# Kernel tuning notes

Measured on AMD Instinct MI355X. Metric: run time of the kernel, lower is better.

Reference implementation:

```python
import jax, jax.numpy as jnp
import numpy as np

B, S, E, FEAT, ATT, NCLS, VOCAB = 32, 512, 512, 256, 10, 8, 32000
# NOTE: original code requires S == E (attentive_content [S,S] assigned into a [S,E] buffer)


def setup_inputs() -> dict:
    key = jax.random.key(0)
    ks = jax.random.split(key, 8)
    x = jax.random.randint(ks[0], (B, S), 0, VOCAB)
    emb = jax.random.normal(ks[1], (VOCAB, E), dtype=jnp.float32) * 0.02
    A = jax.random.uniform(ks[2], (E, ATT), dtype=jnp.float32, minval=-0.1, maxval=0.1)
    Wh = jax.random.normal(ks[3], (FEAT, E, 3), dtype=jnp.float32) * 0.02   # h_conv, k=3, no bias
    Wc = jax.random.normal(ks[4], (FEAT, E), dtype=jnp.float32) * 0.02      # c_conv, k=1, no bias
    tanh_bias = jnp.zeros((FEAT,), dtype=jnp.float32)
    Wfc = jax.random.normal(ks[5], (NCLS, FEAT), dtype=jnp.float32) * 0.02
    bfc = jnp.zeros((NCLS,), dtype=jnp.float32)
    return {"x": x, "emb": emb, "A": A, "Wh": Wh, "Wc": Wc,
            "tanh_bias": tanh_bias, "Wfc": Wfc, "bfc": bfc}


def reference(x, emb, A, Wh, Wc, tanh_bias, Wfc, bfc):
    ex = emb[x]                                    # [B,S,E] embedding lookup
    # batched version of the per-sample loop: mm -> softmax -> mm
    scores = jnp.einsum('bse,ea->bsa', ex, A)      # [B,S,ATT]
    attn = jax.nn.softmax(scores, axis=-1)         # softmax over attention dim (2D default)
    att = jnp.einsum('bsa,bta->bst', attn, scores)  # [B,S,S]  (S == E)
    # h branch: conv1d(k=3, valid) over time, then global max-pool
    h = jax.lax.conv_general_dilated(ex.transpose(0, 2, 1), Wh, (1,), 'VALID',
                                     dimension_numbers=('NCH', 'OIH', 'NCH'))  # [B,F,S-2]
    h = jnp.max(h, axis=-1)                        # [B,F]
    # c branch: k=1 conv over att (permuted), i.e. channel mix, then global max-pool
    c = jnp.max(jnp.einsum('blc,fc->bfl', att, Wc), axis=-1)  # [B,F]
    out = jnp.tanh(h + c + tanh_bias)
    return out @ Wfc.T + bfc                       # [B,num_class]
```

## Files before the change

### kernel.cpp

```cpp
#include <hip/hip_runtime.h>
#include <math.h>

#define B 32
#define S 512
#define E 512
#define FEAT 256
#define ATT 10
#define NCLS 8

using short8 = __attribute__((ext_vector_type(8))) short;
using f32x4  = __attribute__((ext_vector_type(4))) float;

__device__ __forceinline__ unsigned short f2bf(float f) {
    unsigned int u = __float_as_uint(f);
    return (unsigned short)((u + 0x7fffu + ((u >> 16) & 1u)) >> 16);
}

__device__ __forceinline__ void gl16(const void* g, void* l) {
    __builtin_amdgcn_global_load_lds(
        (const __attribute__((address_space(1))) unsigned int*)g,
        (__attribute__((address_space(3))) unsigned int*)l, 16, 0, 0);
}

__global__ __launch_bounds__(256) void k_front(
        const int* __restrict__ x, const float* __restrict__ emb,
        const float* __restrict__ A, const float* __restrict__ Wh,
        unsigned short* __restrict__ ex16, unsigned short* __restrict__ Whk16,
        float* __restrict__ sc12, float* __restrict__ at12) {
    const int blk = blockIdx.x;
    const int tid = threadIdx.x;
    if (blk < 2048) {
        const int wave = tid >> 6, lane = tid & 63;
#pragma unroll
        for (int rep = 0; rep < 2; ++rep) {
            const int bs = blk * 8 + wave * 2 + rep;
            const int row = x[bs];
            const f32x4* src = (const f32x4*)(emb + (size_t)row * E);
            const f32x4 v0 = src[lane * 2], v1 = src[lane * 2 + 1];
            float v[8] = {v0[0], v0[1], v0[2], v0[3], v1[0], v1[1], v1[2], v1[3]};

            short8 sv;
#pragma unroll
            for (int j = 0; j < 8; ++j) sv[j] = (short)f2bf(v[j]);
            *(short8*)(ex16 + (size_t)bs * E + lane * 8) = sv;

            float acc[ATT] = {};
            const float* ap = A + (size_t)lane * 8 * ATT;
#pragma unroll
            for (int j = 0; j < 8; ++j)
#pragma unroll
                for (int a = 0; a < ATT; ++a) acc[a] = fmaf(v[j], ap[j * ATT + a], acc[a]);
#pragma unroll
            for (int a = 0; a < ATT; ++a)
#pragma unroll
                for (int off = 1; off < 64; off <<= 1) acc[a] += __shfl_xor(acc[a], off);

            if (lane == 0) {
                float m = -1e30f;
#pragma unroll
                for (int a = 0; a < ATT; ++a) m = fmaxf(m, acc[a]);
                float ev[ATT], sum = 0.f;
#pragma unroll
                for (int a = 0; a < ATT; ++a) { ev[a] = expf(acc[a] - m); sum += ev[a]; }
                const float inv = 1.f / sum;
                float* sp = sc12 + (size_t)bs * 12;
                float* tp = at12 + (size_t)bs * 12;
                *(f32x4*)(sp)     = (f32x4){acc[0], acc[1], acc[2], acc[3]};
                *(f32x4*)(sp + 4) = (f32x4){acc[4], acc[5], acc[6], acc[7]};
                *(f32x4*)(sp + 8) = (f32x4){acc[8], acc[9], 0.f, 0.f};
                *(f32x4*)(tp)     = (f32x4){ev[0] * inv, ev[1] * inv, ev[2] * inv, ev[3] * inv};
                *(f32x4*)(tp + 4) = (f32x4){ev[4] * inv, ev[5] * inv, ev[6] * inv, ev[7] * inv};
                *(f32x4*)(tp + 8) = (f32x4){ev[8] * inv, ev[9] * inv, 0.f, 0.f};
            }
        }
    } else if (blk < 2048 + FEAT) {
        const int f = blk - 2048;
        const float* src = Wh + (size_t)f * (E * 3);
        unsigned short* dst = Whk16 + (size_t)f * (E * 3);
#pragma unroll
        for (int i = 0; i < 6; ++i) {
            const int kk = tid + i * 256;
            dst[kk] = f2bf(src[(kk & 511) * 3 + (kk >> 9)]);
        }
        if (f == 0) {
            for (int i = tid; i < 2 * E; i += 256) ex16[(size_t)B * S * E + i] = 0;
        }
    }
}

__global__ __launch_bounds__(256) void k_conv(const unsigned short* __restrict__ Whk,
                                              const unsigned short* __restrict__ ex16,
                                              float* __restrict__ Cpart) {
    __shared__ unsigned short lds[3][16384];
    const int b = blockIdx.x;
    const int fbase = blockIdx.y * 128;
    const int lbase = blockIdx.z * 128;
    const int tid = threadIdx.x;
    const int wave = tid >> 6, lane = tid & 63;
    const int wm = wave >> 1, wn = wave & 1;
    const int lane15 = lane & 15, g4 = lane >> 4;
    const int rr = tid >> 3, slot = tid & 7;
    const unsigned short* exb = ex16 + (size_t)b * S * E;

    f32x4 acc[4][4];
#pragma unroll
    for (int mf = 0; mf < 4; ++mf)
#pragma unroll
        for (int nf = 0; nf < 4; ++nf) acc[mf][nf] = (f32x4){0.f, 0.f, 0.f, 0.f};

    auto stage = [&](int t, unsigned short* buf) {
        const int kk0 = t << 6;
        const int kpc = t >> 3;
        const int e0  = (t & 7) << 6;
        unsigned short* la = buf;
        unsigned short* lb = buf + 8192;
#pragma unroll
        for (int i = 0; i < 4; ++i) {
            const int r = i * 32 + rr;
            gl16(Whk + (size_t)(fbase + r) * 1536 + kk0 + ((slot ^ (r & 7)) << 3),
                 la + i * 2048 + wave * 512);
        }
#pragma unroll
        for (int i = 0; i < 4; ++i) {
            const int r = i * 32 + rr;
            gl16(exb + (size_t)(lbase + r + kpc) * E + e0 + ((slot ^ (r & 7)) << 3),
                 lb + i * 2048 + wave * 512);
        }
    };

    auto compute = [&](const unsigned short* buf) {
        const char* la = (const char*)buf;
        const char* lb = (const char*)(buf + 8192);
#pragma unroll
        for (int kh = 0; kh < 2; ++kh) {
            short8 av[4], bv[4];
#pragma unroll
            for (int mf = 0; mf < 4; ++mf) {
                const int row = wm * 64 + mf * 16 + lane15;
                av[mf] = *(const short8*)(la + row * 128 +
                                          ((((kh << 2) | g4) ^ (row & 7)) << 4));
            }
#pragma unroll
            for (int nf = 0; nf < 4; ++nf) {
                const int row = wn * 64 + nf * 16 + lane15;
                bv[nf] = *(const short8*)(lb + row * 128 +
                                          ((((kh << 2) | g4) ^ (row & 7)) << 4));
            }
#pragma unroll
            for (int mf = 0; mf < 4; ++mf)
#pragma unroll
                for (int nf = 0; nf < 4; ++nf)
                    acc[mf][nf] = __builtin_amdgcn_mfma_f32_16x16x32_bf16(
                        av[mf], bv[nf], acc[mf][nf], 0, 0, 0);
        }
    };

    stage(0, lds[0]);
    stage(1, lds[1]);
    asm volatile("s_waitcnt vmcnt(8)" ::: "memory");
    __builtin_amdgcn_s_barrier();

    unsigned short *cur = lds[0], *nxt = lds[1], *nn = lds[2];
    for (int t = 0; t < 24; ++t) {
        if (t + 2 < 24) stage(t + 2, nn);
        compute(cur);
        if (t < 23) {
            if (t + 2 < 24)
                asm volatile("s_waitcnt vmcnt(8)" ::: "memory");
            else
                asm volatile("s_waitcnt vmcnt(0)" ::: "memory");
            __builtin_amdgcn_s_barrier();
        }
        unsigned short* tmp = cur; cur = nxt; nxt = nn; nn = tmp;
    }

#pragma unroll
    for (int mf = 0; mf < 4; ++mf) {
#pragma unroll
        for (int j = 0; j < 4; ++j) {
            float m = -1e30f;
#pragma unroll
            for (int nf = 0; nf < 4; ++nf) {
                const int l = lbase + wn * 64 + nf * 16 + lane15;
                if (l < S - 2) m = fmaxf(m, acc[mf][nf][j]);
            }
#pragma unroll
            for (int off = 1; off < 16; off <<= 1) m = fmaxf(m, __shfl_xor(m, off));
            if (lane15 == 0) {
                const int f = fbase + wm * 64 + mf * 16 + g4 * 4 + j;
                Cpart[(((size_t)b * FEAT + f) << 3) + blockIdx.z * 2 + wn] = m;
            }
        }
    }
}

__global__ __launch_bounds__(256) void k_chc(
        const float* __restrict__ sc12, const float* __restrict__ at12,
        const float* __restrict__ Wc, const float* __restrict__ Cpart,
        const float* __restrict__ tb, float* __restrict__ hc) {
    const int fg = blockIdx.x, b = blockIdx.y;
    const int wave = threadIdx.x >> 6, lane = threadIdx.x & 63;
    const int f0 = fg * 32 + wave * 8;

    f32x4 wc[8][2];
#pragma unroll
    for (int ff = 0; ff < 8; ++ff) {
        const float* wp = Wc + (size_t)(f0 + ff) * E + lane * 8;
        wc[ff][0] = *(const f32x4*)wp;
        wc[ff][1] = *(const f32x4*)(wp + 4);
    }

    f32x4 g[8][3];
#pragma unroll
    for (int ff = 0; ff < 8; ++ff)
#pragma unroll
        for (int q = 0; q < 3; ++q) g[ff][q] = (f32x4){0.f, 0.f, 0.f, 0.f};

    const f32x4* scp = (const f32x4*)(sc12 + (size_t)b * S * 12);
#pragma unroll
    for (int j = 0; j < 8; ++j) {
        const int t = lane * 8 + j;
        const f32x4 s0 = scp[t * 3], s1 = scp[t * 3 + 1], s2 = scp[t * 3 + 2];
#pragma unroll
        for (int ff = 0; ff < 8; ++ff) {
            const float w = wc[ff][j >> 2][j & 3];
            g[ff][0] += s0 * w; g[ff][1] += s1 * w; g[ff][2] += s2 * w;
        }
    }
#pragma unroll
    for (int ff = 0; ff < 8; ++ff)
#pragma unroll
        for (int q = 0; q < 3; ++q)
#pragma unroll
            for (int c = 0; c < 4; ++c)
#pragma unroll
                for (int off = 1; off < 64; off <<= 1)
                    g[ff][q][c] += __shfl_xor(g[ff][q][c], off);

    const f32x4* atp = (const f32x4*)(at12 + (size_t)b * S * 12);
    float mc[8];
#pragma unroll
    for (int ff = 0; ff < 8; ++ff) mc[ff] = -1e30f;
#pragma unroll
    for (int j = 0; j < 8; ++j) {
        const int t = lane * 8 + j;
        const f32x4 a0 = atp[t * 3], a1 = atp[t * 3 + 1], a2 = atp[t * 3 + 2];
#pragma unroll
        for (int ff = 0; ff < 8; ++ff) {
            const f32x4 p = a0 * g[ff][0] + a1 * g[ff][1] + a2 * g[ff][2];
            mc[ff] = fmaxf(mc[ff], p[0] + p[1] + p[2] + p[3]);
        }
    }
#pragma unroll
    for (int ff = 0; ff < 8; ++ff)
#pragma unroll
        for (int off = 1; off < 64; off <<= 1)
            mc[ff] = fmaxf(mc[ff], __shfl_xor(mc[ff], off));

    if (lane == 0) {
#pragma unroll
        for (int ff = 0; ff < 8; ++ff) {
            const int f = f0 + ff;
            const float* cp = Cpart + (((size_t)b * FEAT + f) << 3);
            float mh = cp[0];
#pragma unroll
            for (int q = 1; q < 8; ++q) mh = fmaxf(mh, cp[q]);
            hc[(size_t)b * FEAT + f] = tanhf(mh + mc[ff] + tb[f]);
        }
    }
}

__global__ void k_out(const float* __restrict__ hc, const float* __restrict__ Wfc,
                      const float* __restrict__ bfc, float* __restrict__ out) {
    const int b = blockIdx.x;
    const int tid = threadIdx.x;
    __shared__ float hv[FEAT];
    __shared__ float ps[256];
    hv[tid] = hc[(size_t)b * FEAT + tid];
    __syncthreads();
    const int n = tid & 7;
    const int c = tid >> 3;
    float p = 0.f;
#pragma unroll
    for (int q = 0; q < 8; ++q) p = fmaf(hv[c * 8 + q], Wfc[(size_t)n * FEAT + c * 8 + q], p);
    ps[tid] = p;
    __syncthreads();
    if (tid < 8) {
        float s = bfc[tid];
        for (int q = 0; q < 32; ++q) s += ps[tid + 8 * q];
        out[(size_t)b * NCLS + tid] = s;
    }
}

extern "C" void kernel_launch(void* const* d_in, const int* in_sizes, int n_in,
                              void* d_out, int out_size, void* d_ws, size_t ws_size,
                              hipStream_t stream) {
    const int* x      = (const int*)d_in[0];
    const float* emb  = (const float*)d_in[1];
    const float* A    = (const float*)d_in[2];
    const float* Wh   = (const float*)d_in[3];
    const float* Wc   = (const float*)d_in[4];
    const float* tb   = (const float*)d_in[5];
    const float* Wfc  = (const float*)d_in[6];
    const float* bfc  = (const float*)d_in[7];
    float* out = (float*)d_out;

    unsigned short* ex16  = (unsigned short*)d_ws;
    unsigned short* Whk16 = ex16 + (size_t)B * S * E + 2 * E;
    float* sc12 = (float*)(Whk16 + (size_t)FEAT * 3 * E);
    float* at12 = sc12 + (size_t)B * S * 12;
    float* Cpart = at12 + (size_t)B * S * 12;
    float* hc    = Cpart + (size_t)B * FEAT * 8;

    k_front<<<2048 + FEAT, 256, 0, stream>>>(x, emb, A, Wh, ex16, Whk16, sc12, at12);
    k_conv<<<dim3(B, 2, 4), 256, 0, stream>>>(Whk16, ex16, Cpart);
    k_chc<<<dim3(8, B), 256, 0, stream>>>(sc12, at12, Wc, Cpart, tb, hc);
    k_out<<<B, 256, 0, stream>>>(hc, Wfc, bfc, out);
}
```

Measured before the change: 72.17 us.

## Double K-tile to 128 with two-stage LDS pipeline; cache A in registers

The conv GEMM kernel now loads 128-wide K tiles into two 64KB-per-pair LDS buffers (double buffering), down from 64-wide tiles in a triple-buffered pipeline. This halves the number of loop iterations and barriers, but it reduces prefetch depth and waits for all outstanding loads (vmcnt(0)) before each barrier. The front kernel also preloads each lane's slice of the attention matrix A into registers once, instead of reloading it for each of the two rows it processes. The larger per-block LDS footprint may lower occupancy.

```diff
diff --git a/kernel.cpp b/kernel.cpp
--- a/kernel.cpp
+++ b/kernel.cpp
@@ -31,6 +31,10 @@
     const int tid = threadIdx.x;
     if (blk < 2048) {
         const int wave = tid >> 6, lane = tid & 63;
+        f32x4 av4[20];
+        const f32x4* ap4 = (const f32x4*)(A + (size_t)lane * 80);
+#pragma unroll
+        for (int q = 0; q < 20; ++q) av4[q] = ap4[q];
 #pragma unroll
         for (int rep = 0; rep < 2; ++rep) {
             const int bs = blk * 8 + wave * 2 + rep;
@@ -45,11 +49,13 @@
             *(short8*)(ex16 + (size_t)bs * E + lane * 8) = sv;
 
             float acc[ATT] = {};
-            const float* ap = A + (size_t)lane * 8 * ATT;
 #pragma unroll
             for (int j = 0; j < 8; ++j)
 #pragma unroll
-                for (int a = 0; a < ATT; ++a) acc[a] = fmaf(v[j], ap[j * ATT + a], acc[a]);
+                for (int a = 0; a < ATT; ++a) {
+                    const int idx = j * ATT + a;
+                    acc[a] = fmaf(v[j], av4[idx >> 2][idx & 3], acc[a]);
+                }
 #pragma unroll
             for (int a = 0; a < ATT; ++a)
 #pragma unroll
@@ -91,7 +97,7 @@
 __global__ __launch_bounds__(256) void k_conv(const unsigned short* __restrict__ Whk,
                                               const unsigned short* __restrict__ ex16,
                                               float* __restrict__ Cpart) {
-    __shared__ unsigned short lds[3][16384];
+    __shared__ unsigned short lds[2][32768];
     const int b = blockIdx.x;
     const int fbase = blockIdx.y * 128;
     const int lbase = blockIdx.z * 128;
@@ -99,7 +105,8 @@
     const int wave = tid >> 6, lane = tid & 63;
     const int wm = wave >> 1, wn = wave & 1;
     const int lane15 = lane & 15, g4 = lane >> 4;
-    const int rr = tid >> 3, slot = tid & 7;
+    const int r4 = lane >> 4;
+    const int slot = lane & 15;
     const unsigned short* exb = ex16 + (size_t)b * S * E;
 
     f32x4 acc[4][4];
@@ -109,41 +116,41 @@
         for (int nf = 0; nf < 4; ++nf) acc[mf][nf] = (f32x4){0.f, 0.f, 0.f, 0.f};
 
     auto stage = [&](int t, unsigned short* buf) {
-        const int kk0 = t << 6;
-        const int kpc = t >> 3;
-        const int e0  = (t & 7) << 6;
+        const int kk0 = t << 7;
+        const int kpc = t >> 2;
+        const int e0  = (t & 3) << 7;
         unsigned short* la = buf;
-        unsigned short* lb = buf + 8192;
-#pragma unroll
-        for (int i = 0; i < 4; ++i) {
-            const int r = i * 32 + rr;
+        unsigned short* lb = buf + 16384;
+#pragma unroll
+        for (int ii = 0; ii < 8; ++ii) {
+            const int r = wave * 32 + ii * 4 + r4;
             gl16(Whk + (size_t)(fbase + r) * 1536 + kk0 + ((slot ^ (r & 7)) << 3),
-                 la + i * 2048 + wave * 512);
-        }
-#pragma unroll
-        for (int i = 0; i < 4; ++i) {
-            const int r = i * 32 + rr;
+                 la + (wave * 8 + ii) * 512);
+        }
+#pragma unroll
+        for (int ii = 0; ii < 8; ++ii) {
+            const int r = wave * 32 + ii * 4 + r4;
             gl16(exb + (size_t)(lbase + r + kpc) * E + e0 + ((slot ^ (r & 7)) << 3),
-                 lb + i * 2048 + wave * 512);
+                 lb + (wave * 8 + ii) * 512);
         }
     };
 
     auto compute = [&](const unsigned short* buf) {
         const char* la = (const char*)buf;
-        const char* lb = (const char*)(buf + 8192);
-#pragma unroll
-        for (int kh = 0; kh < 2; ++kh) {
+        const char* lb = (const char*)(buf + 16384);
+#pragma unroll
+        for (int kh = 0; kh < 4; ++kh) {
             short8 av[4], bv[4];
 #pragma unroll
             for (int mf = 0; mf < 4; ++mf) {
                 const int row = wm * 64 + mf * 16 + lane15;
-                av[mf] = *(const short8*)(la + row * 128 +
+                av[mf] = *(const short8*)(la + row * 256 +
                                           ((((kh << 2) | g4) ^ (row & 7)) << 4));
             }
 #pragma unroll
             for (int nf = 0; nf < 4; ++nf) {
                 const int row = wn * 64 + nf * 16 + lane15;
-                bv[nf] = *(const short8*)(lb + row * 128 +
+                bv[nf] = *(const short8*)(lb + row * 256 +
                                           ((((kh << 2) | g4) ^ (row & 7)) << 4));
             }
 #pragma unroll
@@ -156,22 +163,16 @@
     };
 
     stage(0, lds[0]);
-    stage(1, lds[1]);
-    asm volatile("s_waitcnt vmcnt(8)" ::: "memory");
+    asm volatile("s_waitcnt vmcnt(0)" ::: "memory");
     __builtin_amdgcn_s_barrier();
 
-    unsigned short *cur = lds[0], *nxt = lds[1], *nn = lds[2];
-    for (int t = 0; t < 24; ++t) {
-        if (t + 2 < 24) stage(t + 2, nn);
-        compute(cur);
-        if (t < 23) {
-            if (t + 2 < 24)
-                asm volatile("s_waitcnt vmcnt(8)" ::: "memory");
-            else
-                asm volatile("s_waitcnt vmcnt(0)" ::: "memory");
+    for (int t = 0; t < 12; ++t) {
+        if (t + 1 < 12) stage(t + 1, lds[(t + 1) & 1]);
+        compute(lds[t & 1]);
+        if (t + 1 < 12) {
+            asm volatile("s_waitcnt vmcnt(0)" ::: "memory");
             __builtin_amdgcn_s_barrier();
         }
-        unsigned short* tmp = cur; cur = nxt; nxt = nn; nn = tmp;
     }
 
 #pragma unroll
```

New measurement: 66.65 us. 1.08x faster.
